# Optimization experiments

Measured on AMD Instinct MI355X. Metric: run time of the kernel, lower is better.

The kernel has to match this reference:

```python
import jax, jax.numpy as jnp
import numpy as np

N, C_TOTAL, C, H, W = 8, 448, 100, 56, 56


def setup_inputs() -> dict:
    key = jax.random.key(0)
    k1, k2, k3, k4 = jax.random.split(key, 4)
    fmaps = jax.random.normal(k1, (N, C_TOTAL, H, W), dtype=jnp.float32)
    select_index = jax.random.randint(k2, (C,), 0, C_TOTAL)
    mean = jax.random.normal(k3, (C, H, W), dtype=jnp.float32)
    # Per-pixel inverse covariance must be PSD so the quadratic form is >= 0
    A = jax.random.normal(k4, (C, C, H, W), dtype=jnp.float32)
    cov = jnp.einsum('cehw,dehw->cdhw', A, A) / jnp.float32(C)  # (C,C,H,W), PSD per pixel
    return {
        'fmaps': fmaps,
        'select_index': select_index,
        'mean': mean,
        'cov': cov,
        'min_score': jnp.float32(0.0),
        'max_score': jnp.float32(50.0),
    }


def reference(fmaps, select_index, mean, cov, min_score, max_score):
    # x_ = fmaps[:, select_index, ...] - mean  -> (N, C, H, W)
    x = fmaps[:, select_index, :, :] - mean[None]
    # left = sum_c x[n,c,h,w] * cov[c,d,h,w]  (per-pixel matvec), avoids (N,C,C,H,W) intermediate
    left = jnp.einsum('nchw,cdhw->ndhw', x, cov)
    # per-pixel Mahalanobis distance
    s_map = jnp.sqrt(jnp.sum(x * left, axis=1))  # (N, H, W)
    # bilinear upsample x4 (torch Upsample align_corners=False == half-pixel linear resize)
    score_map = jax.image.resize(s_map, (s_map.shape[0], 4 * H, 4 * W), method='linear')
    scores = (score_map - min_score) / (max_score - min_score)
    return jnp.squeeze(scores)
```

## Files before the change

kernel.cpp:

```cpp
#include <hip/hip_runtime.h>
#include <math.h>

#define NN 8
#define C_TOTAL 448
#define CC 100
#define HH 56
#define WW 56
#define HW (HH*WW)
#define NPIX4 (HW/4)
#define OH 224
#define OW 224
#define NPAIR 50
#define NT4 13

typedef __attribute__((ext_vector_type(4))) _Float16 half4;

__device__ __forceinline__ void fma4(float4& acc, const float4 a, const float4 b) {
    acc.x = fmaf(a.x, b.x, acc.x);
    acc.y = fmaf(a.y, b.y, acc.y);
    acc.z = fmaf(a.z, b.z, acc.z);
    acc.w = fmaf(a.w, b.w, acc.w);
}
__device__ __forceinline__ float4 h2f(const half4 h) {
    float4 r; r.x = (float)h.x; r.y = (float)h.y; r.z = (float)h.z; r.w = (float)h.w;
    return r;
}

__global__ __launch_bounds__(256) void prep_x_kernel(
    const float* __restrict__ fmaps, const int* __restrict__ sel,
    const float* __restrict__ mean, half4* __restrict__ xbuf)
{
    const int idx = blockIdx.x * 256 + threadIdx.x;
    if (idx >= CC * NPIX4) return;
    const int quad = idx % NPIX4;
    const int c    = idx / NPIX4;

    const float4* f4 = (const float4*)fmaps;
    const float4  m  = ((const float4*)mean)[(size_t)c * NPIX4 + quad];
    const int     sc = sel[c];

    half4 hv[NN];
#pragma unroll
    for (int n = 0; n < NN; ++n) {
        const float4 f = f4[((size_t)n * C_TOTAL + sc) * NPIX4 + quad];
        half4 h;
        h.x = (_Float16)(f.x - m.x);
        h.y = (_Float16)(f.y - m.y);
        h.z = (_Float16)(f.z - m.z);
        h.w = (_Float16)(f.w - m.w);
        hv[n] = h;
    }
    half4* dst = xbuf + ((size_t)c * NPIX4 + quad) * NN;
#pragma unroll
    for (int n = 0; n < NN; ++n) dst[n] = hv[n];
}

__global__ __launch_bounds__(512, 4) void qform_kernel(
    const half4* __restrict__ xbuf, const float* __restrict__ cov,
    float* __restrict__ qpart)
{
    __shared__ float4 lred[NN * NN * 64];

    const int tile = blockIdx.x % NT4;
    const int r    = blockIdx.x / NT4;
    const int s    = CC - 1 - r;
    const int w    = threadIdx.x >> 6;
    const int lane = threadIdx.x & 63;
    const int qraw = tile * 64 + lane;
    const bool valid = qraw < NPIX4;
    const int quad = valid ? qraw : (NPIX4 - 1);

    const float4* c4 = (const float4*)cov;

    float4 part[NN];
#pragma unroll
    for (int n = 0; n < NN; ++n) part[n] = make_float4(0.f, 0.f, 0.f, 0.f);

    for (int seg = 0; seg < 2; ++seg) {
        const int row = seg ? s : r;

        float4 acc[NN];
#pragma unroll
        for (int n = 0; n < NN; ++n) acc[n] = make_float4(0.f, 0.f, 0.f, 0.f);

        for (int d = row + w; d < CC; d += NN) {
            float4 cv = c4[((size_t)row * CC + d) * NPIX4 + quad];
            if (d == row) { cv.x *= 0.5f; cv.y *= 0.5f; cv.z *= 0.5f; cv.w *= 0.5f; }
            const half4* xp = xbuf + ((size_t)d * NPIX4 + quad) * NN;
            half4 hv[NN];
#pragma unroll
            for (int n = 0; n < NN; ++n) hv[n] = xp[n];
#pragma unroll
            for (int n = 0; n < NN; ++n) fma4(acc[n], h2f(hv[n]), cv);
        }

        const half4* xrp = xbuf + ((size_t)row * NPIX4 + quad) * NN;
#pragma unroll
        for (int n = 0; n < NN; ++n) {
            const float4 xr = h2f(xrp[n]);
            part[n].x = fmaf(2.f * xr.x, acc[n].x, part[n].x);
            part[n].y = fmaf(2.f * xr.y, acc[n].y, part[n].y);
            part[n].z = fmaf(2.f * xr.z, acc[n].z, part[n].z);
            part[n].w = fmaf(2.f * xr.w, acc[n].w, part[n].w);
        }
    }

#pragma unroll
    for (int n = 0; n < NN; ++n) lred[(w * NN + n) * 64 + lane] = part[n];
    __syncthreads();

    {
        const int n = w;
        float4 sum = make_float4(0.f, 0.f, 0.f, 0.f);
#pragma unroll
        for (int ww = 0; ww < NN; ++ww) {
            const float4 v = lred[(ww * NN + n) * 64 + lane];
            sum.x += v.x; sum.y += v.y; sum.z += v.z; sum.w += v.w;
        }
        if (valid) {
            ((float4*)qpart)[((size_t)r * NN + n) * NPIX4 + qraw] = sum;
        }
    }
}

__global__ __launch_bounds__(256) void reduce_kernel(
    const float* __restrict__ qpart, float* __restrict__ smap)
{
    const int idx = blockIdx.x * 256 + threadIdx.x;
    if (idx >= NN * NPIX4) return;
    const int p4 = idx % NPIX4;
    const int n  = idx / NPIX4;

    const float4* qp = (const float4*)qpart;
    float4 acc = make_float4(0.f, 0.f, 0.f, 0.f);
#pragma unroll
    for (int k = 0; k < NPAIR; ++k) {
        const float4 v = qp[((size_t)k * NN + n) * NPIX4 + p4];
        acc.x += v.x; acc.y += v.y; acc.z += v.z; acc.w += v.w;
    }
    float4 o;
    o.x = sqrtf(fmaxf(acc.x, 0.f));
    o.y = sqrtf(fmaxf(acc.y, 0.f));
    o.z = sqrtf(fmaxf(acc.z, 0.f));
    o.w = sqrtf(fmaxf(acc.w, 0.f));
    ((float4*)smap)[(size_t)n * NPIX4 + p4] = o;
}

__global__ __launch_bounds__(256) void upsample_kernel(
    const float* __restrict__ smap,
    const float* __restrict__ minp, const float* __restrict__ maxp,
    float* __restrict__ out)
{
    const int idx = blockIdx.x * 256 + threadIdx.x;
    const int total = NN * OH * OW;
    if (idx >= total) return;

    const int ox = idx % OW;
    const int oy = (idx / OW) % OH;
    const int n  = idx / (OW * OH);

    const float fy = oy * 0.25f - 0.375f;
    const float fx = ox * 0.25f - 0.375f;

    int y0 = (int)floorf(fy);
    int x0 = (int)floorf(fx);
    const float wy = fy - (float)y0;
    const float wx = fx - (float)x0;
    int y1 = min(y0 + 1, HH - 1); y0 = max(y0, 0);
    int x1 = min(x0 + 1, WW - 1); x0 = max(x0, 0);

    const float* s = smap + (size_t)n * HW;
    const float v00 = s[y0 * WW + x0];
    const float v01 = s[y0 * WW + x1];
    const float v10 = s[y1 * WW + x0];
    const float v11 = s[y1 * WW + x1];

    const float v = (1.0f - wy) * ((1.0f - wx) * v00 + wx * v01)
                  +          wy * ((1.0f - wx) * v10 + wx * v11);

    const float mn = *minp;
    const float mx = *maxp;
    out[idx] = (v - mn) / (mx - mn);
}

extern "C" void kernel_launch(void* const* d_in, const int* in_sizes, int n_in,
                              void* d_out, int out_size, void* d_ws, size_t ws_size,
                              hipStream_t stream)
{
    const float* fmaps = (const float*)d_in[0];
    const int*   sel   = (const int*)  d_in[1];
    const float* mean  = (const float*)d_in[2];
    const float* cov   = (const float*)d_in[3];
    const float* minp  = (const float*)d_in[4];
    const float* maxp  = (const float*)d_in[5];
    float* out = (float*)d_out;

    half4* xbuf  = (half4*)d_ws;
    float* qpart = (float*)((char*)d_ws + (size_t)CC*NPIX4*NN*8);
    float* smap  = qpart + (size_t)NPAIR * NN * HW;

    {
        const int total = CC * NPIX4;
        prep_x_kernel<<<(total + 255) / 256, 256, 0, stream>>>(fmaps, sel, mean, xbuf);
    }
    qform_kernel<<<NT4 * NPAIR, 512, 0, stream>>>(xbuf, cov, qpart);
    {
        const int total = NN * NPIX4;
        reduce_kernel<<<(total + 255) / 256, 256, 0, stream>>>(qpart, smap);
    }
    {
        const int total = NN * OH * OW;
        upsample_kernel<<<(total + 255) / 256, 256, 0, stream>>>(smap, minp, maxp, out);
    }
}
```

Baseline: 225.7 us.

## Pair adjacent covariance rows per block and fold reduction into atomics

Each qform block now handles adjacent rows 2k and 2k+1 instead of rows r and 99-r. This lets the shared x loads (now half8 vector loads) feed both rows' accumulators, which reuses x across two covariance rows. The separate reduce kernel and its partials buffer are replaced by atomicAdd into a zeroed smap, with the sqrt moved into the upsample kernel. The cost is worse load balance across blocks, since early row pairs have far more work than late ones, plus atomic contention, non-deterministic summation order, and four extra sqrt calls per output pixel.

```diff
diff --git a/kernel.cpp b/kernel.cpp
--- a/kernel.cpp
+++ b/kernel.cpp
@@ -10,10 +10,11 @@
 #define NPIX4 (HW/4)
 #define OH 224
 #define OW 224
-#define NPAIR 50
 #define NT4 13
+#define NK 50
 
 typedef __attribute__((ext_vector_type(4))) _Float16 half4;
+typedef __attribute__((ext_vector_type(8))) _Float16 half8;
 
 __device__ __forceinline__ void fma4(float4& acc, const float4 a, const float4 b) {
     acc.x = fmaf(a.x, b.x, acc.x);
@@ -28,9 +29,13 @@
 
 __global__ __launch_bounds__(256) void prep_x_kernel(
     const float* __restrict__ fmaps, const int* __restrict__ sel,
-    const float* __restrict__ mean, half4* __restrict__ xbuf)
+    const float* __restrict__ mean, half4* __restrict__ xbuf,
+    float* __restrict__ smap)
 {
     const int idx = blockIdx.x * 256 + threadIdx.x;
+    if (idx < NN * NPIX4) {
+        ((float4*)smap)[idx] = make_float4(0.f, 0.f, 0.f, 0.f);
+    }
     if (idx >= CC * NPIX4) return;
     const int quad = idx % NPIX4;
     const int c    = idx / NPIX4;
@@ -57,13 +62,14 @@
 
 __global__ __launch_bounds__(512, 4) void qform_kernel(
     const half4* __restrict__ xbuf, const float* __restrict__ cov,
-    float* __restrict__ qpart)
+    float* __restrict__ smap)
 {
     __shared__ float4 lred[NN * NN * 64];
 
     const int tile = blockIdx.x % NT4;
-    const int r    = blockIdx.x / NT4;
-    const int s    = CC - 1 - r;
+    const int k    = blockIdx.x / NT4;
+    const int a    = 2 * k;
+    const int b    = a + 1;
     const int w    = threadIdx.x >> 6;
     const int lane = threadIdx.x & 63;
     const int qraw = tile * 64 + lane;
@@ -72,41 +78,55 @@
 
     const float4* c4 = (const float4*)cov;
 
-    float4 part[NN];
-#pragma unroll
-    for (int n = 0; n < NN; ++n) part[n] = make_float4(0.f, 0.f, 0.f, 0.f);
-
-    for (int seg = 0; seg < 2; ++seg) {
-        const int row = seg ? s : r;
-
-        float4 acc[NN];
-#pragma unroll
-        for (int n = 0; n < NN; ++n) acc[n] = make_float4(0.f, 0.f, 0.f, 0.f);
-
-        for (int d = row + w; d < CC; d += NN) {
-            float4 cv = c4[((size_t)row * CC + d) * NPIX4 + quad];
-            if (d == row) { cv.x *= 0.5f; cv.y *= 0.5f; cv.z *= 0.5f; cv.w *= 0.5f; }
-            const half4* xp = xbuf + ((size_t)d * NPIX4 + quad) * NN;
-            half4 hv[NN];
-#pragma unroll
-            for (int n = 0; n < NN; ++n) hv[n] = xp[n];
-#pragma unroll
-            for (int n = 0; n < NN; ++n) fma4(acc[n], h2f(hv[n]), cv);
+    float4 acca[NN], accb[NN];
+#pragma unroll
+    for (int n = 0; n < NN; ++n) {
+        acca[n] = make_float4(0.f, 0.f, 0.f, 0.f);
+        accb[n] = make_float4(0.f, 0.f, 0.f, 0.f);
+    }
+
+    for (int d = a + w; d < CC; d += NN) {
+        const half8* xp = (const half8*)(xbuf + ((size_t)d * NPIX4 + quad) * NN);
+        const half8 p0 = xp[0];
+        const half8 p1 = xp[1];
+        const half8 p2 = xp[2];
+        const half8 p3 = xp[3];
+        float4 xv[NN];
+        xv[0] = make_float4((float)p0[0], (float)p0[1], (float)p0[2], (float)p0[3]);
+        xv[1] = make_float4((float)p0[4], (float)p0[5], (float)p0[6], (float)p0[7]);
+        xv[2] = make_float4((float)p1[0], (float)p1[1], (float)p1[2], (float)p1[3]);
+        xv[3] = make_float4((float)p1[4], (float)p1[5], (float)p1[6], (float)p1[7]);
+        xv[4] = make_float4((float)p2[0], (float)p2[1], (float)p2[2], (float)p2[3]);
+        xv[5] = make_float4((float)p2[4], (float)p2[5], (float)p2[6], (float)p2[7]);
+        xv[6] = make_float4((float)p3[0], (float)p3[1], (float)p3[2], (float)p3[3]);
+        xv[7] = make_float4((float)p3[4], (float)p3[5], (float)p3[6], (float)p3[7]);
+
+        float4 cva = c4[((size_t)a * CC + d) * NPIX4 + quad];
+        if (d == a) { cva.x *= 0.5f; cva.y *= 0.5f; cva.z *= 0.5f; cva.w *= 0.5f; }
+#pragma unroll
+        for (int n = 0; n < NN; ++n) fma4(acca[n], xv[n], cva);
+
+        if (d > a) {
+            float4 cvb = c4[((size_t)b * CC + d) * NPIX4 + quad];
+            if (d == b) { cvb.x *= 0.5f; cvb.y *= 0.5f; cvb.z *= 0.5f; cvb.w *= 0.5f; }
+#pragma unroll
+            for (int n = 0; n < NN; ++n) fma4(accb[n], xv[n], cvb);
         }
-
-        const half4* xrp = xbuf + ((size_t)row * NPIX4 + quad) * NN;
-#pragma unroll
-        for (int n = 0; n < NN; ++n) {
-            const float4 xr = h2f(xrp[n]);
-            part[n].x = fmaf(2.f * xr.x, acc[n].x, part[n].x);
-            part[n].y = fmaf(2.f * xr.y, acc[n].y, part[n].y);
-            part[n].z = fmaf(2.f * xr.z, acc[n].z, part[n].z);
-            part[n].w = fmaf(2.f * xr.w, acc[n].w, part[n].w);
-        }
-    }
-
-#pragma unroll
-    for (int n = 0; n < NN; ++n) lred[(w * NN + n) * 64 + lane] = part[n];
+    }
+
+    const half4* xap = xbuf + ((size_t)a * NPIX4 + quad) * NN;
+    const half4* xbp = xbuf + ((size_t)b * NPIX4 + quad) * NN;
+#pragma unroll
+    for (int n = 0; n < NN; ++n) {
+        const float4 xa = h2f(xap[n]);
+        const float4 xb = h2f(xbp[n]);
+        float4 t;
+        t.x = 2.f * fmaf(xb.x, accb[n].x, xa.x * acca[n].x);
+        t.y = 2.f * fmaf(xb.y, accb[n].y, xa.y * acca[n].y);
+        t.z = 2.f * fmaf(xb.z, accb[n].z, xa.z * acca[n].z);
+        t.w = 2.f * fmaf(xb.w, accb[n].w, xa.w * acca[n].w);
+        lred[(w * NN + n) * 64 + lane] = t;
+    }
     __syncthreads();
 
     {
@@ -118,32 +138,13 @@
             sum.x += v.x; sum.y += v.y; sum.z += v.z; sum.w += v.w;
         }
         if (valid) {
-            ((float4*)qpart)[((size_t)r * NN + n) * NPIX4 + qraw] = sum;
+            float* dst = smap + (size_t)n * HW + (size_t)qraw * 4;
+            atomicAdd(dst + 0, sum.x);
+            atomicAdd(dst + 1, sum.y);
+            atomicAdd(dst + 2, sum.z);
+            atomicAdd(dst + 3, sum.w);
         }
     }
-}
-
-__global__ __launch_bounds__(256) void reduce_kernel(
-    const float* __restrict__ qpart, float* __restrict__ smap)
-{
-    const int idx = blockIdx.x * 256 + threadIdx.x;
-    if (idx >= NN * NPIX4) return;
-    const int p4 = idx % NPIX4;
-    const int n  = idx / NPIX4;
-
-    const float4* qp = (const float4*)qpart;
-    float4 acc = make_float4(0.f, 0.f, 0.f, 0.f);
-#pragma unroll
-    for (int k = 0; k < NPAIR; ++k) {
-        const float4 v = qp[((size_t)k * NN + n) * NPIX4 + p4];
-        acc.x += v.x; acc.y += v.y; acc.z += v.z; acc.w += v.w;
-    }
-    float4 o;
-    o.x = sqrtf(fmaxf(acc.x, 0.f));
-    o.y = sqrtf(fmaxf(acc.y, 0.f));
-    o.z = sqrtf(fmaxf(acc.z, 0.f));
-    o.w = sqrtf(fmaxf(acc.w, 0.f));
-    ((float4*)smap)[(size_t)n * NPIX4 + p4] = o;
 }
 
 __global__ __launch_bounds__(256) void upsample_kernel(
@@ -170,10 +171,10 @@
     int x1 = min(x0 + 1, WW - 1); x0 = max(x0, 0);
 
     const float* s = smap + (size_t)n * HW;
-    const float v00 = s[y0 * WW + x0];
-    const float v01 = s[y0 * WW + x1];
-    const float v10 = s[y1 * WW + x0];
-    const float v11 = s[y1 * WW + x1];
+    const float v00 = sqrtf(fmaxf(s[y0 * WW + x0], 0.f));
+    const float v01 = sqrtf(fmaxf(s[y0 * WW + x1], 0.f));
+    const float v10 = sqrtf(fmaxf(s[y1 * WW + x0], 0.f));
+    const float v11 = sqrtf(fmaxf(s[y1 * WW + x1], 0.f));
 
     const float v = (1.0f - wy) * ((1.0f - wx) * v00 + wx * v01)
                   +          wy * ((1.0f - wx) * v10 + wx * v11);
@@ -195,19 +196,14 @@
     const float* maxp  = (const float*)d_in[5];
     float* out = (float*)d_out;
 
-    half4* xbuf  = (half4*)d_ws;
-    float* qpart = (float*)((char*)d_ws + (size_t)CC*NPIX4*NN*8);
-    float* smap  = qpart + (size_t)NPAIR * NN * HW;
+    half4* xbuf = (half4*)d_ws;
+    float* smap = (float*)((char*)d_ws + (size_t)CC*NPIX4*NN*8);
 
     {
         const int total = CC * NPIX4;
-        prep_x_kernel<<<(total + 255) / 256, 256, 0, stream>>>(fmaps, sel, mean, xbuf);
-    }
-    qform_kernel<<<NT4 * NPAIR, 512, 0, stream>>>(xbuf, cov, qpart);
-    {
-        const int total = NN * NPIX4;
-        reduce_kernel<<<(total + 255) / 256, 256, 0, stream>>>(qpart, smap);
-    }
+        prep_x_kernel<<<(total + 255) / 256, 256, 0, stream>>>(fmaps, sel, mean, xbuf, smap);
+    }
+    qform_kernel<<<NT4 * NK, 512, 0, stream>>>(xbuf, cov, smap);
     {
         const int total = NN * OH * OW;
         upsample_kernel<<<(total + 255) / 256, 256, 0, stream>>>(smap, minp, maxp, out);
```

Result: faster. 216.3 us (-4.2%).
